# Optimization experiments

Hardware: AMD Instinct MI355X
Metric: run time of the kernel (lower is better)

The kernel has to match this reference:

```python
import jax, jax.numpy as jnp
import numpy as np

N = 3072      # nodes
D = 256       # embed_dim
H = 8         # heads
E = 98304     # edges (avg degree 32)
B = 16        # graphs in batch


def setup_inputs() -> dict:
    key = jax.random.key(0)
    ks = jax.random.split(key, 14)
    w = lambda k, sh: jax.random.normal(k, sh, jnp.float32) * 0.02
    return {
        "x": jax.random.normal(ks[0], (N, D), jnp.float32),
        "edge_attr": jax.random.normal(ks[1], (E, 4), jnp.float32),
        "Wq": w(ks[2], (D, D)), "bq": jnp.zeros((D,), jnp.float32),
        "Wk": w(ks[3], (D, D)), "bk": jnp.zeros((D,), jnp.float32),
        "Wv": w(ks[4], (D, D)), "bv": jnp.zeros((D,), jnp.float32),
        "Wo": w(ks[5], (D, D)), "bo": jnp.zeros((D,), jnp.float32),
        "We": w(ks[6], (4, H)), "be": jnp.zeros((H,), jnp.float32),
        "edge_index": jax.random.randint(ks[7], (2, E), 0, N),
        "batch": jnp.sort(jax.random.randint(ks[8], (N,), 0, B)),
    }


def reference(x, edge_attr, Wq, bq, Wk, bk, Wv, bv, Wo, bo, We, be,
              edge_index, batch):
    n, d = x.shape
    h = be.shape[0]
    hd = d // h
    # projections -> [h, n, hd]
    Q = (x @ Wq + bq).reshape(n, h, hd).transpose(1, 0, 2)
    K = (x @ Wk + bk).reshape(n, h, hd).transpose(1, 0, 2)
    V = (x @ Wv + bv).reshape(n, h, hd).transpose(1, 0, 2)
    # dense attention scores [h, n, n]
    scores = jnp.einsum('hnd,hmd->hnm', Q, K) / np.float32(np.sqrt(hd))
    # per-edge bias scatter-add (accumulate over duplicate edges)
    edge_bias = edge_attr @ We + be                     # [E, h]
    scores = scores.at[:, edge_index[0], edge_index[1]].add(edge_bias.T)
    # block-diagonal batch mask
    same_graph = batch[:, None] == batch[None, :]       # [n, n]
    scores = jnp.where(same_graph[None], scores, -jnp.inf)
    attn = jax.nn.softmax(scores, axis=-1)              # dropout: eval mode (identity)
    out = jnp.einsum('hnm,hmd->hnd', attn, V)           # [h, n, hd]
    out = out.transpose(1, 0, 2).reshape(n, d)
    return out @ Wo + bo
```

## Files before the change

kernel.cpp:

```cpp
#include <hip/hip_runtime.h>
#include <hip/hip_bf16.h>
#include <math.h>

#define N_NODES 3072
#define NPAD    3104
#define DIM     256
#define NH      8
#define HD      32
#define E_EDGES 98304
#define B_GRAPHS 16
#define RCAP    96
#define MAXC    332
#define TR      16
#define SCALE   0.17677669529663689f

typedef __attribute__((ext_vector_type(8))) short bf16x8;
typedef __attribute__((ext_vector_type(4))) float f32x4;
typedef __attribute__((ext_vector_type(4))) unsigned short ushort4v;

__device__ inline unsigned short f2b(float f) {
    __hip_bfloat16 h = __float2bfloat16(f);
    return *reinterpret_cast<unsigned short*>(&h);
}
__device__ inline float b2f(unsigned short u) {
    __hip_bfloat16 h = *reinterpret_cast<__hip_bfloat16*>(&u);
    return __bfloat162float(h);
}

__global__ __launch_bounds__(256) void prep(
    const float* __restrict__ x,
    const float* __restrict__ Wq, const float* __restrict__ Wk,
    const float* __restrict__ Wv, const float* __restrict__ Wo,
    const float* __restrict__ ea, const float* __restrict__ We,
    const float* __restrict__ be,
    const int* __restrict__ erow, const int* __restrict__ ecolin,
    unsigned short* __restrict__ xh, unsigned short* __restrict__ xl,
    unsigned short* __restrict__ Wth, unsigned short* __restrict__ Wtl,
    unsigned short* __restrict__ VT, float* __restrict__ ebias,
    const int* __restrict__ batch, int* __restrict__ gstart,
    int* __restrict__ tcur, unsigned int* __restrict__ tbuck)
{
    const int b = blockIdx.x, t = threadIdx.x;
    if (b < 768) {
        const int gid = b * 256 + t;
        float4 v = ((const float4*)x)[gid];
        ushort4v h, l;
        float c[4] = {v.x, v.y, v.z, v.w};
        #pragma unroll
        for (int i = 0; i < 4; ++i) {
            unsigned short hi = f2b(c[i]);
            h[i] = hi;
            l[i] = f2b(c[i] - b2f(hi));
        }
        ((ushort4v*)xh)[gid] = h;
        ((ushort4v*)xl)[gid] = l;
    } else if (b < 1024) {
        __shared__ float tile[32][33];
        const int wb = b - 768;
        const int mat = wb >> 6, tidx = wb & 63;
        const int tk = (tidx >> 3) * 32, tn = (tidx & 7) * 32;
        const float* W = (mat == 0) ? Wq : (mat == 1) ? Wk : (mat == 2) ? Wv : Wo;
        const int kk = t >> 5, nn = t & 31;
        #pragma unroll
        for (int p = 0; p < 4; ++p)
            tile[nn][kk + p * 8] = W[(size_t)(tk + kk + p * 8) * DIM + tn + nn];
        __syncthreads();
        const int n = t >> 3, kq = (t & 7) * 4;
        ushort4v h, l;
        #pragma unroll
        for (int i = 0; i < 4; ++i) {
            float v = tile[n][kq + i];
            unsigned short hi = f2b(v);
            h[i] = hi;
            l[i] = f2b(v - b2f(hi));
        }
        size_t o = (size_t)mat * DIM * DIM + (size_t)(tn + n) * DIM + tk + kq;
        *(ushort4v*)(Wth + o) = h;
        *(ushort4v*)(Wtl + o) = l;
    } else if (b < 1056) {
        const int i = (b - 1024) * 256 + t;
        VT[(size_t)(i >> 5) * NPAD + N_NODES + (i & 31)] = 0;
        if (i < N_NODES) {
            int bb = batch[i];
            int bp = (i == 0) ? -1 : batch[i - 1];
            for (int g = bp + 1; g <= bb; ++g) gstart[g] = i;
            if (i == N_NODES - 1)
                for (int g = bb + 1; g <= B_GRAPHS; ++g) gstart[g] = N_NODES;
        }
    } else {
        const int e = (b - 1056) * 256 + t;
        const int row = erow[e];
        const int col = ecolin[e];
        int pos = atomicAdd(&tcur[row], 1);
        if (pos < RCAP)
            tbuck[(size_t)row * RCAP + pos] = ((unsigned int)e << 12) | (unsigned int)col;
        float4 a = ((const float4*)ea)[e];
        #pragma unroll
        for (int h = 0; h < NH; ++h) {
            float bb = fmaf(a.x, We[0 * NH + h],
                       fmaf(a.y, We[1 * NH + h],
                       fmaf(a.z, We[2 * NH + h],
                       fmaf(a.w, We[3 * NH + h], be[h]))));
            ebias[(size_t)h * E_EDGES + e] = bb;
        }
    }
}

__global__ __launch_bounds__(256) void qkv_mfma(
    const unsigned short* __restrict__ xh, const unsigned short* __restrict__ xl,
    const unsigned short* __restrict__ Wth, const unsigned short* __restrict__ Wtl,
    const float* __restrict__ bq, const float* __restrict__ bk, const float* __restrict__ bv,
    unsigned short* __restrict__ Qb, unsigned short* __restrict__ Kb,
    unsigned short* __restrict__ VT)
{
    const int u = blockIdx.x;
    const int t = threadIdx.x;
    const int w = t >> 6, lane = t & 63;
    const int l16 = lane & 15, lq = lane >> 4;
    const int bx = u % 96, by = u / 96;
    const int mat = by >> 2;
    const int rb = bx * 32 + (w & 1) * 16;
    const int nb = (by & 3) * 64 + (w >> 1) * 32;
    const unsigned short* Wh = Wth + (size_t)mat * DIM * DIM;
    const unsigned short* Wl = Wtl + (size_t)mat * DIM * DIM;

    f32x4 acc[2] = {{0,0,0,0},{0,0,0,0}};

    if (mat < 2) {
        const size_t arow = (size_t)(rb + l16) * DIM + (lq << 3);
        #pragma unroll
        for (int kc = 0; kc < 8; ++kc) {
            const int k = kc * 32;
            bf16x8 ah = *(const bf16x8*)(xh + arow + k);
            bf16x8 al = *(const bf16x8*)(xl + arow + k);
            #pragma unroll
            for (int ct = 0; ct < 2; ++ct) {
                const size_t bo_ = (size_t)(nb + ct * 16 + l16) * DIM + k + (lq << 3);
                bf16x8 bh = *(const bf16x8*)(Wh + bo_);
                bf16x8 bl = *(const bf16x8*)(Wl + bo_);
                acc[ct] = __builtin_amdgcn_mfma_f32_16x16x32_bf16(ah, bh, acc[ct], 0, 0, 0);
                acc[ct] = __builtin_amdgcn_mfma_f32_16x16x32_bf16(ah, bl, acc[ct], 0, 0, 0);
                acc[ct] = __builtin_amdgcn_mfma_f32_16x16x32_bf16(al, bh, acc[ct], 0, 0, 0);
            }
        }
        const float* bias = (mat == 0) ? bq : bk;
        unsigned short* outp = (mat == 0) ? Qb : Kb;
        #pragma unroll
        for (int ct = 0; ct < 2; ++ct) {
            const int n = nb + ct * 16 + l16;
            const float bvl = bias[n];
            #pragma unroll
            for (int r = 0; r < 4; ++r)
                outp[(size_t)(rb + lq * 4 + r) * DIM + n] = f2b(acc[ct][r] + bvl);
        }
    } else {
        const size_t brow = (size_t)(rb + l16) * DIM + (lq << 3);
        #pragma unroll
        for (int kc = 0; kc < 8; ++kc) {
            const int k = kc * 32;
            bf16x8 bxh = *(const bf16x8*)(xh + brow + k);
            bf16x8 bxl = *(const bf16x8*)(xl + brow + k);
            #pragma unroll
            for (int ct = 0; ct < 2; ++ct) {
                const size_t ao_ = (size_t)(nb + ct * 16 + l16) * DIM + k + (lq << 3);
                bf16x8 awh = *(const bf16x8*)(Wh + ao_);
                bf16x8 awl = *(const bf16x8*)(Wl + ao_);
                acc[ct] = __builtin_amdgcn_mfma_f32_16x16x32_bf16(awh, bxh, acc[ct], 0, 0, 0);
                acc[ct] = __builtin_amdgcn_mfma_f32_16x16x32_bf16(awh, bxl, acc[ct], 0, 0, 0);
                acc[ct] = __builtin_amdgcn_mfma_f32_16x16x32_bf16(awl, bxh, acc[ct], 0, 0, 0);
            }
        }
        #pragma unroll
        for (int ct = 0; ct < 2; ++ct) {
            #pragma unroll
            for (int r = 0; r < 4; ++r) {
                const int ncol = nb + ct * 16 + lq * 4 + r;
                VT[(size_t)ncol * NPAD + rb + l16] = f2b(acc[ct][r] + bv[ncol]);
            }
        }
    }
}

__global__ __launch_bounds__(256) void attn(
    const unsigned short* __restrict__ Qb, const unsigned short* __restrict__ Kb,
    const unsigned short* __restrict__ VT,
    const int* __restrict__ gstart,
    const int* __restrict__ tcur, const unsigned int* __restrict__ tbuck,
    const float* __restrict__ ebias,
    unsigned short* __restrict__ preh, unsigned short* __restrict__ prel)
{
    __shared__ __align__(16) float s[TR][MAXC];
    __shared__ float rowinv[TR];

    const int g = blockIdx.x, tile = blockIdx.y, h = blockIdx.z;
    const int gs = gstart[g], ge = gstart[g + 1];
    const int row0 = gs + tile * TR;
    if (row0 >= ge) return;
    const int nrows = min(TR, ge - row0);
    const int ncols = ge - gs;
    const int ags   = gs & ~15;
    const int coff  = gs - ags;
    const int tcols = coff + ncols;
    const int cpad  = (tcols + 31) & ~31;
    const int t = threadIdx.x;
    const int wave = t >> 6, lane = t & 63;
    const int l16 = lane & 15, lq = lane >> 4;

    {
        int arow = min(row0 + l16, N_NODES - 1);
        const bf16x8 aq = *(const bf16x8*)(Qb + (size_t)arow * DIM + h * HD + (lq << 3));
        const int nchunk16 = (tcols + 15) >> 4;
        for (int j = wave; j < nchunk16; j += 4) {
            const int c0 = j << 4;
            int krow = min(ags + c0 + l16, N_NODES - 1);
            bf16x8 bk = *(const bf16x8*)(Kb + (size_t)krow * DIM + h * HD + (lq << 3));
            f32x4 d = {0.f, 0.f, 0.f, 0.f};
            d = __builtin_amdgcn_mfma_f32_16x16x32_bf16(aq, bk, d, 0, 0, 0);
            const int col = c0 + l16, rbase = lq * 4;
            #pragma unroll
            for (int r = 0; r < 4; ++r) s[rbase + r][col] = d[r] * SCALE;
        }
    }
    __syncthreads();

    {
        const int r = t >> 4, sub = t & 15;
        if (r < nrows) {
            const int cnt = min(tcur[row0 + r], RCAP);
            const unsigned int* bk = tbuck + (size_t)(row0 + r) * RCAP;
            for (int idx = sub; idx < cnt; idx += 16) {
                unsigned int p = bk[idx];
                int c = (int)(p & 0xFFFu) - gs;
                if (c >= 0 && c < ncols)
                    atomicAdd(&s[r][coff + c], ebias[(size_t)h * E_EDGES + (p >> 12)]);
            }
        }
    }
    __syncthreads();

    {
        const int r = t >> 4, sub = t & 15;
        if (r < nrows) {
            float m = -INFINITY;
            for (int c = coff + sub; c < tcols; c += 16) m = fmaxf(m, s[r][c]);
            m = fmaxf(m, __shfl_xor(m, 1, 16));
            m = fmaxf(m, __shfl_xor(m, 2, 16));
            m = fmaxf(m, __shfl_xor(m, 4, 16));
            m = fmaxf(m, __shfl_xor(m, 8, 16));
            float sum = 0.f;
            for (int c = sub; c < cpad; c += 16) {
                float e = 0.f;
                if (c >= coff && c < tcols) e = __expf(s[r][c] - m);
                sum += e;
                s[r][c] = e;
            }
            sum += __shfl_xor(sum, 1, 16);
            sum += __shfl_xor(sum, 2, 16);
            sum += __shfl_xor(sum, 4, 16);
            sum += __shfl_xor(sum, 8, 16);
            if (sub == 0) rowinv[r] = 1.0f / sum;
        } else {
            for (int c = sub; c < cpad; c += 16) s[r][c] = 0.f;
        }
    }
    __syncthreads();

    f32x4 o = {0.f, 0.f, 0.f, 0.f};
    {
        const int half = wave >> 1, par = wave & 1;
        const int kout = l16 + (half << 4);
        const int nchunk32 = cpad >> 5;
        const unsigned short* vrow = VT + (size_t)(h * HD + kout) * NPAD + ags + (lq << 3);
        for (int j = par; j < nchunk32; j += 2) {
            const int c0 = j << 5;
            const float4 p0 = *(const float4*)&s[l16][c0 + (lq << 3)];
            const float4 p1 = *(const float4*)&s[l16][c0 + (lq << 3) + 4];
            bf16x8 ap;
            ap[0] = f2b(p0.x); ap[1] = f2b(p0.y); ap[2] = f2b(p0.z); ap[3] = f2b(p0.w);
            ap[4] = f2b(p1.x); ap[5] = f2b(p1.y); ap[6] = f2b(p1.z); ap[7] = f2b(p1.w);
            bf16x8 bv = *(const bf16x8*)(vrow + c0);
            o = __builtin_amdgcn_mfma_f32_16x16x32_bf16(ap, bv, o, 0, 0, 0);
        }
    }
    __syncthreads();
    {
        float* red = &s[0][0];
        const int rbase = lq * 4;
        #pragma unroll
        for (int r = 0; r < 4; ++r)
            red[((wave << 4) + rbase + r) * 17 + l16] = o[r];
    }
    __syncthreads();
    {
        const int row = t >> 4, kl = t & 15;
        if (row < nrows) {
            float* red = &s[0][0];
            float v0 = red[(row) * 17 + kl]        + red[(16 + row) * 17 + kl];
            float v1 = red[(32 + row) * 17 + kl]   + red[(48 + row) * 17 + kl];
            float sc = rowinv[row];
            size_t ob = (size_t)(row0 + row) * DIM + h * HD;
            float f0 = v0 * sc, f1 = v1 * sc;
            unsigned short h0 = f2b(f0), h1 = f2b(f1);
            preh[ob + kl]      = h0;
            preh[ob + 16 + kl] = h1;
            prel[ob + kl]      = f2b(f0 - b2f(h0));
            prel[ob + 16 + kl] = f2b(f1 - b2f(h1));
        }
    }
}

__global__ __launch_bounds__(256) void out_mfma(
    const unsigned short* __restrict__ preh, const unsigned short* __restrict__ prel,
    const unsigned short* __restrict__ Wth, const unsigned short* __restrict__ Wtl,
    const float* __restrict__ bo, float* __restrict__ out)
{
    const int t = threadIdx.x, w = t >> 6, lane = t & 63;
    const int l16 = lane & 15, lq = lane >> 4;
    const int rb = blockIdx.x * 16;
    const int nb = blockIdx.y * 128 + w * 32;
    const unsigned short* Wh = Wth + (size_t)3 * DIM * DIM;
    const unsigned short* Wl = Wtl + (size_t)3 * DIM * DIM;

    f32x4 acc[2] = {{0,0,0,0},{0,0,0,0}};
    const size_t arow = (size_t)(rb + l16) * DIM + (lq << 3);

    #pragma unroll
    for (int kc = 0; kc < 8; ++kc) {
        const int k = kc * 32;
        bf16x8 ah = *(const bf16x8*)(preh + arow + k);
        bf16x8 al = *(const bf16x8*)(prel + arow + k);
        #pragma unroll
        for (int ct = 0; ct < 2; ++ct) {
            const size_t bo_ = (size_t)(nb + ct * 16 + l16) * DIM + k + (lq << 3);
            bf16x8 bh = *(const bf16x8*)(Wh + bo_);
            bf16x8 bl = *(const bf16x8*)(Wl + bo_);
            acc[ct] = __builtin_amdgcn_mfma_f32_16x16x32_bf16(ah, bh, acc[ct], 0, 0, 0);
            acc[ct] = __builtin_amdgcn_mfma_f32_16x16x32_bf16(ah, bl, acc[ct], 0, 0, 0);
            acc[ct] = __builtin_amdgcn_mfma_f32_16x16x32_bf16(al, bh, acc[ct], 0, 0, 0);
        }
    }

    #pragma unroll
    for (int ct = 0; ct < 2; ++ct) {
        const int n = nb + ct * 16 + l16;
        const float bvl = bo[n];
        #pragma unroll
        for (int r = 0; r < 4; ++r)
            out[(size_t)(rb + lq * 4 + r) * DIM + n] = acc[ct][r] + bvl;
    }
}

extern "C" void kernel_launch(void* const* d_in, const int* in_sizes, int n_in,
                              void* d_out, int out_size, void* d_ws, size_t ws_size,
                              hipStream_t stream) {
    const float* x   = (const float*)d_in[0];
    const float* ea  = (const float*)d_in[1];
    const float* Wq  = (const float*)d_in[2];  const float* bq = (const float*)d_in[3];
    const float* Wk  = (const float*)d_in[4];  const float* bk = (const float*)d_in[5];
    const float* Wv  = (const float*)d_in[6];  const float* bv = (const float*)d_in[7];
    const float* Wo  = (const float*)d_in[8];  const float* bo = (const float*)d_in[9];
    const float* We  = (const float*)d_in[10]; const float* be = (const float*)d_in[11];
    const int*   eidx  = (const int*)d_in[12];
    const int*   batch = (const int*)d_in[13];
    const int* erow   = eidx;
    const int* ecolin = eidx + E_EDGES;

    const size_t ND = (size_t)N_NODES * DIM;
    const size_t WD = (size_t)DIM * DIM;

    unsigned short* Qb   = (unsigned short*)d_ws;
    unsigned short* Kb   = Qb + ND;
    unsigned short* VT   = Kb + ND;
    unsigned short* preh = VT + (size_t)DIM * NPAD;
    unsigned short* prel = preh + ND;
    unsigned short* xh   = prel + ND;
    unsigned short* xl   = xh + ND;
    unsigned short* Wth  = xl + ND;
    unsigned short* Wtl  = Wth + 4 * WD;
    unsigned int* tbuck  = (unsigned int*)(Wtl + 4 * WD);
    float* ebias  = (float*)(tbuck + (size_t)N_NODES * RCAP);
    int* tcur     = (int*)(ebias + (size_t)NH * E_EDGES);
    int* gstart   = tcur + N_NODES;

    hipMemsetAsync(tcur, 0, N_NODES * sizeof(int), stream);
    prep<<<dim3(1440), dim3(256), 0, stream>>>(x, Wq, Wk, Wv, Wo, ea, We, be,
                                               erow, ecolin, xh, xl, Wth, Wtl,
                                               VT, ebias, batch, gstart, tcur, tbuck);
    qkv_mfma<<<dim3(1152), dim3(256), 0, stream>>>(xh, xl, Wth, Wtl, bq, bk, bv,
                                                   Qb, Kb, VT);
    attn<<<dim3(B_GRAPHS, 24, NH), dim3(256), 0, stream>>>(Qb, Kb, VT, gstart,
                                                           tcur, tbuck, ebias, preh, prel);
    out_mfma<<<dim3(192, 2), dim3(256), 0, stream>>>(preh, prel, Wth, Wtl, bo, (float*)d_out);
}
```

Baseline: 158.3 us.

## Fuse all stages into one persistent cooperative kernel with grid syncs

Result: slower. 366.4 us (+131.4%).

```diff
diff --git a/kernel.cpp b/kernel.cpp
--- a/kernel.cpp
+++ b/kernel.cpp
@@ -1,6 +1,9 @@
 #include <hip/hip_runtime.h>
+#include <hip/hip_cooperative_groups.h>
 #include <hip/hip_bf16.h>
 #include <math.h>
+
+namespace cg = cooperative_groups;
 
 #define N_NODES 3072
 #define NPAD    3104
@@ -27,94 +30,93 @@
     return __bfloat162float(h);
 }
 
-__global__ __launch_bounds__(256) void prep(
-    const float* __restrict__ x,
-    const float* __restrict__ Wq, const float* __restrict__ Wk,
-    const float* __restrict__ Wv, const float* __restrict__ Wo,
-    const float* __restrict__ ea, const float* __restrict__ We,
-    const float* __restrict__ be,
-    const int* __restrict__ erow, const int* __restrict__ ecolin,
-    unsigned short* __restrict__ xh, unsigned short* __restrict__ xl,
-    unsigned short* __restrict__ Wth, unsigned short* __restrict__ Wtl,
-    unsigned short* __restrict__ VT, float* __restrict__ ebias,
-    const int* __restrict__ batch, int* __restrict__ gstart,
-    int* __restrict__ tcur, unsigned int* __restrict__ tbuck)
-{
-    const int b = blockIdx.x, t = threadIdx.x;
-    if (b < 768) {
-        const int gid = b * 256 + t;
-        float4 v = ((const float4*)x)[gid];
-        ushort4v h, l;
-        float c[4] = {v.x, v.y, v.z, v.w};
-        #pragma unroll
-        for (int i = 0; i < 4; ++i) {
-            unsigned short hi = f2b(c[i]);
-            h[i] = hi;
-            l[i] = f2b(c[i] - b2f(hi));
-        }
-        ((ushort4v*)xh)[gid] = h;
-        ((ushort4v*)xl)[gid] = l;
-    } else if (b < 1024) {
-        __shared__ float tile[32][33];
-        const int wb = b - 768;
-        const int mat = wb >> 6, tidx = wb & 63;
-        const int tk = (tidx >> 3) * 32, tn = (tidx & 7) * 32;
-        const float* W = (mat == 0) ? Wq : (mat == 1) ? Wk : (mat == 2) ? Wv : Wo;
-        const int kk = t >> 5, nn = t & 31;
-        #pragma unroll
-        for (int p = 0; p < 4; ++p)
-            tile[nn][kk + p * 8] = W[(size_t)(tk + kk + p * 8) * DIM + tn + nn];
-        __syncthreads();
-        const int n = t >> 3, kq = (t & 7) * 4;
-        ushort4v h, l;
-        #pragma unroll
-        for (int i = 0; i < 4; ++i) {
-            float v = tile[n][kq + i];
-            unsigned short hi = f2b(v);
-            h[i] = hi;
-            l[i] = f2b(v - b2f(hi));
-        }
-        size_t o = (size_t)mat * DIM * DIM + (size_t)(tn + n) * DIM + tk + kq;
-        *(ushort4v*)(Wth + o) = h;
-        *(ushort4v*)(Wtl + o) = l;
-    } else if (b < 1056) {
-        const int i = (b - 1024) * 256 + t;
-        VT[(size_t)(i >> 5) * NPAD + N_NODES + (i & 31)] = 0;
-        if (i < N_NODES) {
-            int bb = batch[i];
-            int bp = (i == 0) ? -1 : batch[i - 1];
-            for (int g = bp + 1; g <= bb; ++g) gstart[g] = i;
-            if (i == N_NODES - 1)
-                for (int g = bb + 1; g <= B_GRAPHS; ++g) gstart[g] = N_NODES;
-        }
-    } else {
-        const int e = (b - 1056) * 256 + t;
-        const int row = erow[e];
-        const int col = ecolin[e];
-        int pos = atomicAdd(&tcur[row], 1);
-        if (pos < RCAP)
-            tbuck[(size_t)row * RCAP + pos] = ((unsigned int)e << 12) | (unsigned int)col;
-        float4 a = ((const float4*)ea)[e];
-        #pragma unroll
-        for (int h = 0; h < NH; ++h) {
-            float bb = fmaf(a.x, We[0 * NH + h],
-                       fmaf(a.y, We[1 * NH + h],
-                       fmaf(a.z, We[2 * NH + h],
-                       fmaf(a.w, We[3 * NH + h], be[h]))));
-            ebias[(size_t)h * E_EDGES + e] = bb;
-        }
-    }
-}
-
-__global__ __launch_bounds__(256) void qkv_mfma(
-    const unsigned short* __restrict__ xh, const unsigned short* __restrict__ xl,
-    const unsigned short* __restrict__ Wth, const unsigned short* __restrict__ Wtl,
-    const float* __restrict__ bq, const float* __restrict__ bk, const float* __restrict__ bv,
-    unsigned short* __restrict__ Qb, unsigned short* __restrict__ Kb,
-    unsigned short* __restrict__ VT)
-{
-    const int u = blockIdx.x;
-    const int t = threadIdx.x;
+
+__device__ inline void xsplit_body(int u, int t, const float* __restrict__ x,
+                                   unsigned short* __restrict__ xh,
+                                   unsigned short* __restrict__ xl) {
+    const int gid = u * 256 + t;
+    float4 v = ((const float4*)x)[gid];
+    ushort4v h, l;
+    float c[4] = {v.x, v.y, v.z, v.w};
+    #pragma unroll
+    for (int i = 0; i < 4; ++i) {
+        unsigned short hi = f2b(c[i]);
+        h[i] = hi;
+        l[i] = f2b(c[i] - b2f(hi));
+    }
+    ((ushort4v*)xh)[gid] = h;
+    ((ushort4v*)xl)[gid] = l;
+}
+
+__device__ inline void wtrans_body(int wb, int t,
+                                   const float* __restrict__ Wq, const float* __restrict__ Wk,
+                                   const float* __restrict__ Wv, const float* __restrict__ Wo,
+                                   unsigned short* __restrict__ Wth,
+                                   unsigned short* __restrict__ Wtl,
+                                   float (*tile)[33]) {
+    const int mat = wb >> 6, tidx = wb & 63;
+    const int tk = (tidx >> 3) * 32, tn = (tidx & 7) * 32;
+    const float* W = (mat == 0) ? Wq : (mat == 1) ? Wk : (mat == 2) ? Wv : Wo;
+    const int kk = t >> 5, nn = t & 31;
+    #pragma unroll
+    for (int p = 0; p < 4; ++p)
+        tile[nn][kk + p * 8] = W[(size_t)(tk + kk + p * 8) * DIM + tn + nn];
+    __syncthreads();
+    const int n = t >> 3, kq = (t & 7) * 4;
+    ushort4v h, l;
+    #pragma unroll
+    for (int i = 0; i < 4; ++i) {
+        float v = tile[n][kq + i];
+        unsigned short hi = f2b(v);
+        h[i] = hi;
+        l[i] = f2b(v - b2f(hi));
+    }
+    size_t o = (size_t)mat * DIM * DIM + (size_t)(tn + n) * DIM + tk + kq;
+    *(ushort4v*)(Wth + o) = h;
+    *(ushort4v*)(Wtl + o) = l;
+}
+
+__device__ inline void vtpad_body(int i, const int* __restrict__ batch,
+                                  unsigned short* __restrict__ VT,
+                                  int* __restrict__ gstart) {
+    VT[(size_t)(i >> 5) * NPAD + N_NODES + (i & 31)] = 0;
+    if (i < N_NODES) {
+        int bb = batch[i];
+        int bp = (i == 0) ? -1 : batch[i - 1];
+        for (int g = bp + 1; g <= bb; ++g) gstart[g] = i;
+        if (i == N_NODES - 1)
+            for (int g = bb + 1; g <= B_GRAPHS; ++g) gstart[g] = N_NODES;
+    }
+}
+
+__device__ inline void edge_body(int e, const float* __restrict__ ea,
+                                 const float* __restrict__ We, const float* __restrict__ be,
+                                 const int* __restrict__ erow, const int* __restrict__ ecolin,
+                                 float* __restrict__ ebias, int* __restrict__ tcur,
+                                 unsigned int* __restrict__ tbuck) {
+    const int row = erow[e];
+    const int col = ecolin[e];
+    int pos = atomicAdd(&tcur[row], 1);
+    if (pos < RCAP)
+        tbuck[(size_t)row * RCAP + pos] = ((unsigned int)e << 12) | (unsigned int)col;
+    float4 a = ((const float4*)ea)[e];
+    #pragma unroll
+    for (int h = 0; h < NH; ++h) {
+        float bb = fmaf(a.x, We[0 * NH + h],
+                   fmaf(a.y, We[1 * NH + h],
+                   fmaf(a.z, We[2 * NH + h],
+                   fmaf(a.w, We[3 * NH + h], be[h]))));
+        ebias[(size_t)h * E_EDGES + e] = bb;
+    }
+}
+
+__device__ inline void qkv_body(int u, int t,
+                                const unsigned short* __restrict__ xh, const unsigned short* __restrict__ xl,
+                                const unsigned short* __restrict__ Wth, const unsigned short* __restrict__ Wtl,
+                                const float* __restrict__ bq, const float* __restrict__ bk,
+                                const float* __restrict__ bv,
+                                unsigned short* __restrict__ Qb, unsigned short* __restrict__ Kb,
+                                unsigned short* __restrict__ VT) {
     const int w = t >> 6, lane = t & 63;
     const int l16 = lane & 15, lq = lane >> 4;
     const int bx = u % 96, by = u / 96;
@@ -181,20 +183,19 @@
     }
 }
 
-__global__ __launch_bounds__(256) void attn(
-    const unsigned short* __restrict__ Qb, const unsigned short* __restrict__ Kb,
-    const unsigned short* __restrict__ VT,
-    const int* __restrict__ gstart,
-    const int* __restrict__ tcur, const unsigned int* __restrict__ tbuck,
-    const float* __restrict__ ebias,
-    unsigned short* __restrict__ preh, unsigned short* __restrict__ prel)
-{
-    __shared__ __align__(16) float s[TR][MAXC];
-    __shared__ float rowinv[TR];
-
-    const int g = blockIdx.x, tile = blockIdx.y, h = blockIdx.z;
+__device__ inline void attn_body(int g, int tile_, int h, int t,
+                                 const unsigned short* __restrict__ Qb,
+                                 const unsigned short* __restrict__ Kb,
+                                 const unsigned short* __restrict__ VT,
+                                 const int* __restrict__ gstart,
+                                 const int* __restrict__ tcur,
+                                 const unsigned int* __restrict__ tbuck,
+                                 const float* __restrict__ ebias,
+                                 unsigned short* __restrict__ preh,
+                                 unsigned short* __restrict__ prel,
+                                 float (*s)[MAXC], float* rowinv) {
     const int gs = gstart[g], ge = gstart[g + 1];
-    const int row0 = gs + tile * TR;
+    const int row0 = gs + tile_ * TR;
     if (row0 >= ge) return;
     const int nrows = min(TR, ge - row0);
     const int ncols = ge - gs;
@@ -202,7 +203,6 @@
     const int coff  = gs - ags;
     const int tcols = coff + ncols;
     const int cpad  = (tcols + 31) & ~31;
-    const int t = threadIdx.x;
     const int wave = t >> 6, lane = t & 63;
     const int l16 = lane & 15, lq = lane >> 4;
 
@@ -309,15 +309,16 @@
     }
 }
 
-__global__ __launch_bounds__(256) void out_mfma(
-    const unsigned short* __restrict__ preh, const unsigned short* __restrict__ prel,
-    const unsigned short* __restrict__ Wth, const unsigned short* __restrict__ Wtl,
-    const float* __restrict__ bo, float* __restrict__ out)
-{
-    const int t = threadIdx.x, w = t >> 6, lane = t & 63;
+__device__ inline void out_body(int bxo, int byo, int t,
+                                const unsigned short* __restrict__ preh,
+                                const unsigned short* __restrict__ prel,
+                                const unsigned short* __restrict__ Wth,
+                                const unsigned short* __restrict__ Wtl,
+                                const float* __restrict__ bo, float* __restrict__ out) {
+    const int w = t >> 6, lane = t & 63;
     const int l16 = lane & 15, lq = lane >> 4;
-    const int rb = blockIdx.x * 16;
-    const int nb = blockIdx.y * 128 + w * 32;
+    const int rb = bxo * 16;
+    const int nb = byo * 128 + w * 32;
     const unsigned short* Wh = Wth + (size_t)3 * DIM * DIM;
     const unsigned short* Wl = Wtl + (size_t)3 * DIM * DIM;
 
@@ -348,6 +349,121 @@
         for (int r = 0; r < 4; ++r)
             out[(size_t)(rb + lq * 4 + r) * DIM + n] = acc[ct][r] + bvl;
     }
+}
+
+__global__ __launch_bounds__(256, 4) void mega(
+    const float* __restrict__ x,
+    const float* __restrict__ Wq, const float* __restrict__ Wk,
+    const float* __restrict__ Wv, const float* __restrict__ Wo,
+    const float* __restrict__ ea, const float* __restrict__ We,
+    const float* __restrict__ be,
+    const int* __restrict__ erow, const int* __restrict__ ecolin,
+    const float* __restrict__ bq, const float* __restrict__ bk,
+    const float* __restrict__ bv, const float* __restrict__ bo,
+    const int* __restrict__ batch,
+    unsigned short* __restrict__ xh, unsigned short* __restrict__ xl,
+    unsigned short* __restrict__ Wth, unsigned short* __restrict__ Wtl,
+    unsigned short* __restrict__ Qb, unsigned short* __restrict__ Kb,
+    unsigned short* __restrict__ VT, unsigned short* __restrict__ preh,
+    unsigned short* __restrict__ prel,
+    float* __restrict__ ebias, int* __restrict__ gstart,
+    int* __restrict__ tcur, unsigned int* __restrict__ tbuck,
+    float* __restrict__ out)
+{
+    cg::grid_group grid = cg::this_grid();
+    __shared__ __align__(16) float smem[TR * MAXC + TR];
+    const int t = threadIdx.x;
+    const int G = gridDim.x;
+
+    for (int u = blockIdx.x; u < 1068; u += G) {
+        if (u < 768) {
+            xsplit_body(u, t, x, xh, xl);
+        } else if (u < 1024) {
+            wtrans_body(u - 768, t, Wq, Wk, Wv, Wo, Wth, Wtl, (float(*)[33])smem);
+            __syncthreads();
+        } else if (u < 1056) {
+            vtpad_body((u - 1024) * 256 + t, batch, VT, gstart);
+        } else {
+            tcur[(u - 1056) * 256 + t] = 0;
+        }
+    }
+    grid.sync();
+
+    for (int u = blockIdx.x; u < 1536; u += G) {
+        if (u < 384) edge_body(u * 256 + t, ea, We, be, erow, ecolin, ebias, tcur, tbuck);
+        else         qkv_body(u - 384, t, xh, xl, Wth, Wtl, bq, bk, bv, Qb, Kb, VT);
+    }
+    grid.sync();
+
+    {
+        float (*s)[MAXC] = (float(*)[MAXC])smem;
+        float* rowinv = smem + TR * MAXC;
+        for (int u = blockIdx.x; u < 3072; u += G) {
+            const int g = u & 15, r2 = u >> 4;
+            attn_body(g, r2 % 24, r2 / 24, t, Qb, Kb, VT, gstart, tcur, tbuck,
+                      ebias, preh, prel, s, rowinv);
+            __syncthreads();
+        }
+    }
+    grid.sync();
+
+    for (int u = blockIdx.x; u < 384; u += G)
+        out_body(u % 192, u / 192, t, preh, prel, Wth, Wtl, bo, out);
+}
+
+
+__global__ __launch_bounds__(256) void prep(
+    const float* __restrict__ x,
+    const float* __restrict__ Wq, const float* __restrict__ Wk,
+    const float* __restrict__ Wv, const float* __restrict__ Wo,
+    const float* __restrict__ ea, const float* __restrict__ We,
+    const float* __restrict__ be,
+    const int* __restrict__ erow, const int* __restrict__ ecolin,
+    unsigned short* __restrict__ xh, unsigned short* __restrict__ xl,
+    unsigned short* __restrict__ Wth, unsigned short* __restrict__ Wtl,
+    unsigned short* __restrict__ VT, float* __restrict__ ebias,
+    const int* __restrict__ batch, int* __restrict__ gstart,
+    int* __restrict__ tcur, unsigned int* __restrict__ tbuck)
+{
+    __shared__ float tile[32][33];
+    const int b = blockIdx.x, t = threadIdx.x;
+    if (b < 768)        xsplit_body(b, t, x, xh, xl);
+    else if (b < 1024)  wtrans_body(b - 768, t, Wq, Wk, Wv, Wo, Wth, Wtl, tile);
+    else if (b < 1056)  vtpad_body((b - 1024) * 256 + t, batch, VT, gstart);
+    else                edge_body((b - 1056) * 256 + t, ea, We, be, erow, ecolin,
+                                  ebias, tcur, tbuck);
+}
+
+__global__ __launch_bounds__(256) void qkv_mfma(
+    const unsigned short* __restrict__ xh, const unsigned short* __restrict__ xl,
+    const unsigned short* __restrict__ Wth, const unsigned short* __restrict__ Wtl,
+    const float* __restrict__ bq, const float* __restrict__ bk, const float* __restrict__ bv,
+    unsigned short* __restrict__ Qb, unsigned short* __restrict__ Kb,
+    unsigned short* __restrict__ VT)
+{
+    qkv_body(blockIdx.x, threadIdx.x, xh, xl, Wth, Wtl, bq, bk, bv, Qb, Kb, VT);
+}
+
+__global__ __launch_bounds__(256) void attn(
+    const unsigned short* __restrict__ Qb, const unsigned short* __restrict__ Kb,
+    const unsigned short* __restrict__ VT,
+    const int* __restrict__ gstart,
+    const int* __restrict__ tcur, const unsigned int* __restrict__ tbuck,
+    const float* __restrict__ ebias,
+    unsigned short* __restrict__ preh, unsigned short* __restrict__ prel)
+{
+    __shared__ __align__(16) float s[TR][MAXC];
+    __shared__ float rowinv[TR];
+    attn_body(blockIdx.x, blockIdx.y, blockIdx.z, threadIdx.x,
+              Qb, Kb, VT, gstart, tcur, tbuck, ebias, preh, prel, s, rowinv);
+}
+
+__global__ __launch_bounds__(256) void out_mfma(
+    const unsigned short* __restrict__ preh, const unsigned short* __restrict__ prel,
+    const unsigned short* __restrict__ Wth, const unsigned short* __restrict__ Wtl,
+    const float* __restrict__ bo, float* __restrict__ out)
+{
+    out_body(blockIdx.x, blockIdx.y, threadIdx.x, preh, prel, Wth, Wtl, bo, out);
 }
 
 extern "C" void kernel_launch(void* const* d_in, const int* in_sizes, int n_in,
@@ -364,6 +480,7 @@
     const int*   batch = (const int*)d_in[13];
     const int* erow   = eidx;
     const int* ecolin = eidx + E_EDGES;
+    float* outp = (float*)d_out;
 
     const size_t ND = (size_t)N_NODES * DIM;
     const size_t WD = (size_t)DIM * DIM;
@@ -382,6 +499,33 @@
     int* tcur     = (int*)(ebias + (size_t)NH * E_EDGES);
     int* gstart   = tcur + N_NODES;
 
+    static int coopBlocks = -2;
+    if (coopBlocks == -2) {
+        int mb = 0;
+        if (hipOccupancyMaxActiveBlocksPerMultiprocessor(&mb, mega, 256, 0) == hipSuccess
+            && mb > 0) {
+            coopBlocks = mb * 256;
+            if (coopBlocks > 3072) coopBlocks = 3072;
+        } else {
+            coopBlocks = 0;
+        }
+    }
+
+    if (coopBlocks > 0) {
+        void* args[] = {
+            (void*)&x, (void*)&Wq, (void*)&Wk, (void*)&Wv, (void*)&Wo,
+            (void*)&ea, (void*)&We, (void*)&be, (void*)&erow, (void*)&ecolin,
+            (void*)&bq, (void*)&bk, (void*)&bv, (void*)&bo, (void*)&batch,
+            (void*)&xh, (void*)&xl, (void*)&Wth, (void*)&Wtl,
+            (void*)&Qb, (void*)&Kb, (void*)&VT, (void*)&preh, (void*)&prel,
+            (void*)&ebias, (void*)&gstart, (void*)&tcur, (void*)&tbuck, (void*)&outp
+        };
+        hipError_t e = hipLaunchCooperativeKernel(mega, dim3(coopBlocks), dim3(256),
+                                                  args, 0, stream);
+        if (e == hipSuccess) return;
+        coopBlocks = 0;
+    }
+
     hipMemsetAsync(tcur, 0, N_NODES * sizeof(int), stream);
     prep<<<dim3(1440), dim3(256), 0, stream>>>(x, Wq, Wk, Wv, Wo, ea, We, be,
                                                erow, ecolin, xh, xl, Wth, Wtl,
@@ -390,5 +534,5 @@
                                                    Qb, Kb, VT);
     attn<<<dim3(B_GRAPHS, 24, NH), dim3(256), 0, stream>>>(Qb, Kb, VT, gstart,
                                                            tcur, tbuck, ebias, preh, prel);
-    out_mfma<<<dim3(192, 2), dim3(256), 0, stream>>>(preh, prel, Wth, Wtl, bo, (float*)d_out);
-}
+    out_mfma<<<dim3(192, 2), dim3(256), 0, stream>>>(preh, prel, Wth, Wtl, bo, outp);
+}
```

## Replace memset with in-kernel zeroing and co-schedule edge prep with QKV GEMM

Applied to the files above, without the earlier changes.

Result: faster. 154.6 us (-2.4%).

```diff
diff --git a/kernel.cpp b/kernel.cpp
--- a/kernel.cpp
+++ b/kernel.cpp
@@ -27,94 +27,93 @@
     return __bfloat162float(h);
 }
 
-__global__ __launch_bounds__(256) void prep(
-    const float* __restrict__ x,
-    const float* __restrict__ Wq, const float* __restrict__ Wk,
-    const float* __restrict__ Wv, const float* __restrict__ Wo,
-    const float* __restrict__ ea, const float* __restrict__ We,
-    const float* __restrict__ be,
-    const int* __restrict__ erow, const int* __restrict__ ecolin,
-    unsigned short* __restrict__ xh, unsigned short* __restrict__ xl,
-    unsigned short* __restrict__ Wth, unsigned short* __restrict__ Wtl,
-    unsigned short* __restrict__ VT, float* __restrict__ ebias,
-    const int* __restrict__ batch, int* __restrict__ gstart,
-    int* __restrict__ tcur, unsigned int* __restrict__ tbuck)
-{
-    const int b = blockIdx.x, t = threadIdx.x;
-    if (b < 768) {
-        const int gid = b * 256 + t;
-        float4 v = ((const float4*)x)[gid];
-        ushort4v h, l;
-        float c[4] = {v.x, v.y, v.z, v.w};
-        #pragma unroll
-        for (int i = 0; i < 4; ++i) {
-            unsigned short hi = f2b(c[i]);
-            h[i] = hi;
-            l[i] = f2b(c[i] - b2f(hi));
-        }
-        ((ushort4v*)xh)[gid] = h;
-        ((ushort4v*)xl)[gid] = l;
-    } else if (b < 1024) {
-        __shared__ float tile[32][33];
-        const int wb = b - 768;
-        const int mat = wb >> 6, tidx = wb & 63;
-        const int tk = (tidx >> 3) * 32, tn = (tidx & 7) * 32;
-        const float* W = (mat == 0) ? Wq : (mat == 1) ? Wk : (mat == 2) ? Wv : Wo;
-        const int kk = t >> 5, nn = t & 31;
-        #pragma unroll
-        for (int p = 0; p < 4; ++p)
-            tile[nn][kk + p * 8] = W[(size_t)(tk + kk + p * 8) * DIM + tn + nn];
-        __syncthreads();
-        const int n = t >> 3, kq = (t & 7) * 4;
-        ushort4v h, l;
-        #pragma unroll
-        for (int i = 0; i < 4; ++i) {
-            float v = tile[n][kq + i];
-            unsigned short hi = f2b(v);
-            h[i] = hi;
-            l[i] = f2b(v - b2f(hi));
-        }
-        size_t o = (size_t)mat * DIM * DIM + (size_t)(tn + n) * DIM + tk + kq;
-        *(ushort4v*)(Wth + o) = h;
-        *(ushort4v*)(Wtl + o) = l;
-    } else if (b < 1056) {
-        const int i = (b - 1024) * 256 + t;
-        VT[(size_t)(i >> 5) * NPAD + N_NODES + (i & 31)] = 0;
-        if (i < N_NODES) {
-            int bb = batch[i];
-            int bp = (i == 0) ? -1 : batch[i - 1];
-            for (int g = bp + 1; g <= bb; ++g) gstart[g] = i;
-            if (i == N_NODES - 1)
-                for (int g = bb + 1; g <= B_GRAPHS; ++g) gstart[g] = N_NODES;
-        }
-    } else {
-        const int e = (b - 1056) * 256 + t;
-        const int row = erow[e];
-        const int col = ecolin[e];
-        int pos = atomicAdd(&tcur[row], 1);
-        if (pos < RCAP)
-            tbuck[(size_t)row * RCAP + pos] = ((unsigned int)e << 12) | (unsigned int)col;
-        float4 a = ((const float4*)ea)[e];
-        #pragma unroll
-        for (int h = 0; h < NH; ++h) {
-            float bb = fmaf(a.x, We[0 * NH + h],
-                       fmaf(a.y, We[1 * NH + h],
-                       fmaf(a.z, We[2 * NH + h],
-                       fmaf(a.w, We[3 * NH + h], be[h]))));
-            ebias[(size_t)h * E_EDGES + e] = bb;
-        }
-    }
-}
-
-__global__ __launch_bounds__(256) void qkv_mfma(
-    const unsigned short* __restrict__ xh, const unsigned short* __restrict__ xl,
-    const unsigned short* __restrict__ Wth, const unsigned short* __restrict__ Wtl,
-    const float* __restrict__ bq, const float* __restrict__ bk, const float* __restrict__ bv,
-    unsigned short* __restrict__ Qb, unsigned short* __restrict__ Kb,
-    unsigned short* __restrict__ VT)
-{
-    const int u = blockIdx.x;
-    const int t = threadIdx.x;
+
+__device__ inline void xsplit_body(int u, int t, const float* __restrict__ x,
+                                   unsigned short* __restrict__ xh,
+                                   unsigned short* __restrict__ xl) {
+    const int gid = u * 256 + t;
+    float4 v = ((const float4*)x)[gid];
+    ushort4v h, l;
+    float c[4] = {v.x, v.y, v.z, v.w};
+    #pragma unroll
+    for (int i = 0; i < 4; ++i) {
+        unsigned short hi = f2b(c[i]);
+        h[i] = hi;
+        l[i] = f2b(c[i] - b2f(hi));
+    }
+    ((ushort4v*)xh)[gid] = h;
+    ((ushort4v*)xl)[gid] = l;
+}
+
+__device__ inline void wtrans_body(int wb, int t,
+                                   const float* __restrict__ Wq, const float* __restrict__ Wk,
+                                   const float* __restrict__ Wv, const float* __restrict__ Wo,
+                                   unsigned short* __restrict__ Wth,
+                                   unsigned short* __restrict__ Wtl,
+                                   float (*tile)[33]) {
+    const int mat = wb >> 6, tidx = wb & 63;
+    const int tk = (tidx >> 3) * 32, tn = (tidx & 7) * 32;
+    const float* W = (mat == 0) ? Wq : (mat == 1) ? Wk : (mat == 2) ? Wv : Wo;
+    const int kk = t >> 5, nn = t & 31;
+    #pragma unroll
+    for (int p = 0; p < 4; ++p)
+        tile[nn][kk + p * 8] = W[(size_t)(tk + kk + p * 8) * DIM + tn + nn];
+    __syncthreads();
+    const int n = t >> 3, kq = (t & 7) * 4;
+    ushort4v h, l;
+    #pragma unroll
+    for (int i = 0; i < 4; ++i) {
+        float v = tile[n][kq + i];
+        unsigned short hi = f2b(v);
+        h[i] = hi;
+        l[i] = f2b(v - b2f(hi));
+    }
+    size_t o = (size_t)mat * DIM * DIM + (size_t)(tn + n) * DIM + tk + kq;
+    *(ushort4v*)(Wth + o) = h;
+    *(ushort4v*)(Wtl + o) = l;
+}
+
+__device__ inline void vtpad_body(int i, const int* __restrict__ batch,
+                                  unsigned short* __restrict__ VT,
+                                  int* __restrict__ gstart) {
+    VT[(size_t)(i >> 5) * NPAD + N_NODES + (i & 31)] = 0;
+    if (i < N_NODES) {
+        int bb = batch[i];
+        int bp = (i == 0) ? -1 : batch[i - 1];
+        for (int g = bp + 1; g <= bb; ++g) gstart[g] = i;
+        if (i == N_NODES - 1)
+            for (int g = bb + 1; g <= B_GRAPHS; ++g) gstart[g] = N_NODES;
+    }
+}
+
+__device__ inline void edge_body(int e, const float* __restrict__ ea,
+                                 const float* __restrict__ We, const float* __restrict__ be,
+                                 const int* __restrict__ erow, const int* __restrict__ ecolin,
+                                 float* __restrict__ ebias, int* __restrict__ tcur,
+                                 unsigned int* __restrict__ tbuck) {
+    const int row = erow[e];
+    const int col = ecolin[e];
+    int pos = atomicAdd(&tcur[row], 1);
+    if (pos < RCAP)
+        tbuck[(size_t)row * RCAP + pos] = ((unsigned int)e << 12) | (unsigned int)col;
+    float4 a = ((const float4*)ea)[e];
+    #pragma unroll
+    for (int h = 0; h < NH; ++h) {
+        float bb = fmaf(a.x, We[0 * NH + h],
+                   fmaf(a.y, We[1 * NH + h],
+                   fmaf(a.z, We[2 * NH + h],
+                   fmaf(a.w, We[3 * NH + h], be[h]))));
+        ebias[(size_t)h * E_EDGES + e] = bb;
+    }
+}
+
+__device__ inline void qkv_body(int u, int t,
+                                const unsigned short* __restrict__ xh, const unsigned short* __restrict__ xl,
+                                const unsigned short* __restrict__ Wth, const unsigned short* __restrict__ Wtl,
+                                const float* __restrict__ bq, const float* __restrict__ bk,
+                                const float* __restrict__ bv,
+                                unsigned short* __restrict__ Qb, unsigned short* __restrict__ Kb,
+                                unsigned short* __restrict__ VT) {
     const int w = t >> 6, lane = t & 63;
     const int l16 = lane & 15, lq = lane >> 4;
     const int bx = u % 96, by = u / 96;
@@ -181,20 +180,19 @@
     }
 }
 
-__global__ __launch_bounds__(256) void attn(
-    const unsigned short* __restrict__ Qb, const unsigned short* __restrict__ Kb,
-    const unsigned short* __restrict__ VT,
-    const int* __restrict__ gstart,
-    const int* __restrict__ tcur, const unsigned int* __restrict__ tbuck,
-    const float* __restrict__ ebias,
-    unsigned short* __restrict__ preh, unsigned short* __restrict__ prel)
-{
-    __shared__ __align__(16) float s[TR][MAXC];
-    __shared__ float rowinv[TR];
-
-    const int g = blockIdx.x, tile = blockIdx.y, h = blockIdx.z;
+__device__ inline void attn_body(int g, int tile_, int h, int t,
+                                 const unsigned short* __restrict__ Qb,
+                                 const unsigned short* __restrict__ Kb,
+                                 const unsigned short* __restrict__ VT,
+                                 const int* __restrict__ gstart,
+                                 const int* __restrict__ tcur,
+                                 const unsigned int* __restrict__ tbuck,
+                                 const float* __restrict__ ebias,
+                                 unsigned short* __restrict__ preh,
+                                 unsigned short* __restrict__ prel,
+                                 float (*s)[MAXC], float* rowinv) {
     const int gs = gstart[g], ge = gstart[g + 1];
-    const int row0 = gs + tile * TR;
+    const int row0 = gs + tile_ * TR;
     if (row0 >= ge) return;
     const int nrows = min(TR, ge - row0);
     const int ncols = ge - gs;
@@ -202,7 +200,6 @@
     const int coff  = gs - ags;
     const int tcols = coff + ncols;
     const int cpad  = (tcols + 31) & ~31;
-    const int t = threadIdx.x;
     const int wave = t >> 6, lane = t & 63;
     const int l16 = lane & 15, lq = lane >> 4;
 
@@ -309,15 +306,16 @@
     }
 }
 
-__global__ __launch_bounds__(256) void out_mfma(
-    const unsigned short* __restrict__ preh, const unsigned short* __restrict__ prel,
-    const unsigned short* __restrict__ Wth, const unsigned short* __restrict__ Wtl,
-    const float* __restrict__ bo, float* __restrict__ out)
-{
-    const int t = threadIdx.x, w = t >> 6, lane = t & 63;
+__device__ inline void out_body(int bxo, int byo, int t,
+                                const unsigned short* __restrict__ preh,
+                                const unsigned short* __restrict__ prel,
+                                const unsigned short* __restrict__ Wth,
+                                const unsigned short* __restrict__ Wtl,
+                                const float* __restrict__ bo, float* __restrict__ out) {
+    const int w = t >> 6, lane = t & 63;
     const int l16 = lane & 15, lq = lane >> 4;
-    const int rb = blockIdx.x * 16;
-    const int nb = blockIdx.y * 128 + w * 32;
+    const int rb = bxo * 16;
+    const int nb = byo * 128 + w * 32;
     const unsigned short* Wh = Wth + (size_t)3 * DIM * DIM;
     const unsigned short* Wl = Wtl + (size_t)3 * DIM * DIM;
 
@@ -348,6 +346,63 @@
         for (int r = 0; r < 4; ++r)
             out[(size_t)(rb + lq * 4 + r) * DIM + n] = acc[ct][r] + bvl;
     }
+}
+
+__global__ __launch_bounds__(256) void prep_a(
+    const float* __restrict__ x,
+    const float* __restrict__ Wq, const float* __restrict__ Wk,
+    const float* __restrict__ Wv, const float* __restrict__ Wo,
+    unsigned short* __restrict__ xh, unsigned short* __restrict__ xl,
+    unsigned short* __restrict__ Wth, unsigned short* __restrict__ Wtl,
+    int* __restrict__ tcur)
+{
+    __shared__ float tile[32][33];
+    const int b = blockIdx.x, t = threadIdx.x;
+    if (b < 768)        xsplit_body(b, t, x, xh, xl);
+    else if (b < 1024)  wtrans_body(b - 768, t, Wq, Wk, Wv, Wo, Wth, Wtl, tile);
+    else                tcur[(b - 1024) * 256 + t] = 0;
+}
+
+__global__ __launch_bounds__(256) void stage2(
+    const unsigned short* __restrict__ xh, const unsigned short* __restrict__ xl,
+    const unsigned short* __restrict__ Wth, const unsigned short* __restrict__ Wtl,
+    const float* __restrict__ bq, const float* __restrict__ bk,
+    const float* __restrict__ bv,
+    const float* __restrict__ ea, const float* __restrict__ We,
+    const float* __restrict__ be,
+    const int* __restrict__ erow, const int* __restrict__ ecolin,
+    const int* __restrict__ batch,
+    unsigned short* __restrict__ Qb, unsigned short* __restrict__ Kb,
+    unsigned short* __restrict__ VT,
+    float* __restrict__ ebias, int* __restrict__ gstart,
+    int* __restrict__ tcur, unsigned int* __restrict__ tbuck)
+{
+    const int b = blockIdx.x, t = threadIdx.x;
+    if (b < 384)        edge_body(b * 256 + t, ea, We, be, erow, ecolin, ebias, tcur, tbuck);
+    else if (b < 1536)  qkv_body(b - 384, t, xh, xl, Wth, Wtl, bq, bk, bv, Qb, Kb, VT);
+    else                vtpad_body((b - 1536) * 256 + t, batch, VT, gstart);
+}
+
+__global__ __launch_bounds__(256) void attn(
+    const unsigned short* __restrict__ Qb, const unsigned short* __restrict__ Kb,
+    const unsigned short* __restrict__ VT,
+    const int* __restrict__ gstart,
+    const int* __restrict__ tcur, const unsigned int* __restrict__ tbuck,
+    const float* __restrict__ ebias,
+    unsigned short* __restrict__ preh, unsigned short* __restrict__ prel)
+{
+    __shared__ __align__(16) float s[TR][MAXC];
+    __shared__ float rowinv[TR];
+    attn_body(blockIdx.x, blockIdx.y, blockIdx.z, threadIdx.x,
+              Qb, Kb, VT, gstart, tcur, tbuck, ebias, preh, prel, s, rowinv);
+}
+
+__global__ __launch_bounds__(256) void out_mfma(
+    const unsigned short* __restrict__ preh, const unsigned short* __restrict__ prel,
+    const unsigned short* __restrict__ Wth, const unsigned short* __restrict__ Wtl,
+    const float* __restrict__ bo, float* __restrict__ out)
+{
+    out_body(blockIdx.x, blockIdx.y, threadIdx.x, preh, prel, Wth, Wtl, bo, out);
 }
 
 extern "C" void kernel_launch(void* const* d_in, const int* in_sizes, int n_in,
@@ -382,12 +437,11 @@
     int* tcur     = (int*)(ebias + (size_t)NH * E_EDGES);
     int* gstart   = tcur + N_NODES;
 
-    hipMemsetAsync(tcur, 0, N_NODES * sizeof(int), stream);
-    prep<<<dim3(1440), dim3(256), 0, stream>>>(x, Wq, Wk, Wv, Wo, ea, We, be,
-                                               erow, ecolin, xh, xl, Wth, Wtl,
-                                               VT, ebias, batch, gstart, tcur, tbuck);
-    qkv_mfma<<<dim3(1152), dim3(256), 0, stream>>>(xh, xl, Wth, Wtl, bq, bk, bv,
-                                                   Qb, Kb, VT);
+    prep_a<<<dim3(1036), dim3(256), 0, stream>>>(x, Wq, Wk, Wv, Wo,
+                                                 xh, xl, Wth, Wtl, tcur);
+    stage2<<<dim3(1568), dim3(256), 0, stream>>>(xh, xl, Wth, Wtl, bq, bk, bv,
+                                                 ea, We, be, erow, ecolin, batch,
+                                                 Qb, Kb, VT, ebias, gstart, tcur, tbuck);
     attn<<<dim3(B_GRAPHS, 24, NH), dim3(256), 0, stream>>>(Qb, Kb, VT, gstart,
                                                            tcur, tbuck, ebias, preh, prel);
     out_mfma<<<dim3(192, 2), dim3(256), 0, stream>>>(preh, prel, Wth, Wtl, bo, (float*)d_out);
```
